# Kernel optimization log

Hardware: AMD Instinct MI355X
Metric: run time of the kernel (lower is better)

Reference implementation:

```python
import jax, jax.numpy as jnp
import numpy as np

B, L, D, H, P = 8, 1024, 128, 128, 8
W = 2 * L  # total words
FT = 0.1   # forget-gate floor


def _lin_init(k, out_d, in_d):
    k1, k2 = jax.random.split(k)
    s = 1.0 / np.sqrt(in_d)
    Wm = jax.random.uniform(k1, (out_d, in_d), minval=-s, maxval=s, dtype=jnp.float32)
    b = jax.random.uniform(k2, (out_d,), minval=-s, maxval=s, dtype=jnp.float32)
    return Wm, b


def setup_inputs() -> dict:
    key = jax.random.key(0)
    ks = jax.random.split(key, 32)
    inp = {
        "word_span0": jax.random.normal(ks[0], (B, L, D), dtype=jnp.float32),
        "word_span1": jax.random.normal(ks[1], (B, L, D), dtype=jnp.float32),
        "node_hidden": jax.random.normal(ks[2], (B, D), dtype=jnp.float32),
        "op_embedding": jax.random.normal(ks[3], (B, P, D), dtype=jnp.float32),
        "word_exist_sequence": jax.random.uniform(ks[4], (B, W), dtype=jnp.float32),
        "word_exist_matrix": jax.random.uniform(ks[5], (B, W, W), dtype=jnp.float32),
        "word_operator": jax.random.uniform(ks[6], (B, W, P), dtype=jnp.float32),
        "word_word": jax.random.uniform(ks[7], (B, W, W), dtype=jnp.float32),
        "depend0": jax.random.uniform(ks[8], (B, L, L), dtype=jnp.float32),
        "depend1": jax.random.uniform(ks[9], (B, L, L), dtype=jnp.float32),
        "goal_word": jax.random.uniform(ks[10], (B, W), dtype=jnp.float32),
    }
    dims = [("w_w_s", H, D), ("w_w_k", H, D), ("w_update", D, 3 * H),
            ("g_w", H, D), ("w_o", D, D), ("b2u_forget", D, 3 * H + D),
            ("b2u_forget2", D, 2 * D), ("linear_output", D, D),
            ("o_w", H, D), ("w_g", D, D), ("u2b_forget", D, 2 * D),
            ("w_o_forget", P, D + P * D), ("w_o_rel", P, D + P * D),
            ("w_o_update", P, 2 * P)]
    for i, (nm, o, ii) in enumerate(dims):
        Wm, b = _lin_init(ks[11 + i], o, ii)
        inp[nm + "_W"] = Wm
        inp[nm + "_b"] = b
    return inp


def _lin(x, Wm, b):
    return x @ Wm.T + b


def _nrm(m):
    # row-normalize by count of nonzero entries (torch normalize_matrix)
    return m / ((m != 0).sum(-1, keepdims=True).astype(m.dtype) + 1e-30)


def _l2(x):
    return x / (jnp.linalg.norm(x, axis=-1, keepdims=True) + 1e-30)


def _hgcn(span0, span1, node_hidden, op_emb, wes, wem, w_op, ww, dep0, dep1, gw, p):
    # ---- Bottom2Up ----
    all_word = jnp.concatenate([span0, span1], axis=1)              # [B,W,D]
    goal_trans = _lin(node_hidden, p["g_w_W"], p["g_w_b"])[:, None, :]  # [B,1,H]
    word_g = _l2(goal_trans * gw[..., None])                        # [B,W,H]
    wk_trans = _lin(all_word, p["w_w_k_W"], p["w_w_k_b"])           # [B,W,H]
    word_w_k = _l2(_nrm(ww * wem) @ wk_trans)                       # [B,W,H]
    word_w_s = _l2(jnp.concatenate(
        [_nrm(dep0) @ _lin(span0, p["w_w_s_W"], p["w_w_s_b"]),
         _nrm(dep1) @ _lin(span1, p["w_w_s_W"], p["w_w_s_b"])], axis=1))
    neighbor = jnp.concatenate([word_g, word_w_k, word_w_s], axis=-1)  # [B,W,3H]
    forget = jax.nn.sigmoid(_lin(jnp.concatenate([all_word, word_g, word_w_k, word_w_s], axis=-1),
                                 p["b2u_forget_W"], p["b2u_forget_b"]))
    word_updated = jnp.clip(forget, FT) * all_word + (1 - forget) * jax.nn.relu(
        _lin(neighbor, p["w_update_W"], p["w_update_b"]))           # [B,W,D]
    word_op = _nrm(jnp.swapaxes(wes[..., None] * w_op, 1, 2)) @ _lin(
        word_updated, p["w_o_W"], p["w_o_b"])                       # [B,P,D]
    forget2 = jax.nn.sigmoid(_lin(jnp.concatenate([op_emb, word_op], axis=-1),
                                  p["b2u_forget2_W"], p["b2u_forget2_b"]))
    op_emb = jnp.clip(forget2, FT) * op_emb + (1 - forget2) * jax.nn.relu(
        _lin(word_op, p["linear_output_W"], p["linear_output_b"]))  # [B,P,D]

    # ---- update_graph ----
    awe_n = _l2(word_updated)
    op_n = _l2(op_emb).reshape(op_emb.shape[0], -1)                 # [B,P*D]
    concate = jnp.concatenate(
        [awe_n, jnp.broadcast_to(op_n[:, None, :], (awe_n.shape[0], awe_n.shape[1], op_n.shape[-1]))],
        axis=-1)                                                    # [B,W,D+P*D]
    fg = jnp.clip(jax.nn.sigmoid(_lin(concate, p["w_o_forget_W"], p["w_o_forget_b"])), FT)
    upd = jax.nn.softmax(jax.nn.relu(_lin(
        jnp.concatenate([w_op, _lin(concate, p["w_o_rel_W"], p["w_o_rel_b"])], axis=-1),
        p["w_o_update_W"], p["w_o_update_b"])), axis=-1)
    w_op_new = fg * w_op + (1 - fg) * upd                           # [B,W,P]

    # ---- Up2Bottom ----
    span0u, span1u = word_updated[:, :L], word_updated[:, L:]
    word_o = _l2(w_op_new @ _lin(op_emb, p["o_w_W"], p["o_w_b"]))   # [B,W,H]
    word_w_k2 = _l2(_nrm(ww * wem) @ _lin(word_updated, p["w_w_k_W"], p["w_w_k_b"]))
    word_w_s2 = _l2(jnp.concatenate(
        [_nrm(dep0) @ _lin(span0u, p["w_w_s_W"], p["w_w_s_b"]),
         _nrm(dep1) @ _lin(span1u, p["w_w_s_W"], p["w_w_s_b"])], axis=1))
    neighbor2 = jnp.concatenate([word_o, word_w_k2, word_w_s2], axis=-1)
    word_updated2 = jax.nn.relu(_lin(neighbor2, p["w_update_W"], p["w_update_b"]))  # [B,W,D]
    goal_w = jnp.einsum('bw,bwd->bd', _nrm(gw * wes), word_updated2)  # [B,D]
    goal_updated = jax.nn.relu(_lin(goal_w, p["w_g_W"], p["w_g_b"]))
    fg3 = jax.nn.sigmoid(_lin(jnp.concatenate([goal_w, node_hidden], axis=-1),
                              p["u2b_forget_W"], p["u2b_forget_b"]))
    goal_next = jnp.clip(fg3, FT) * node_hidden + (1 - fg3) * goal_updated
    return (span0u, span1u, op_emb, goal_next)


def reference(word_span0, word_span1, node_hidden, op_embedding, word_exist_sequence,
              word_exist_matrix, word_operator, word_word, depend0, depend1, goal_word,
              w_w_s_W, w_w_s_b, w_w_k_W, w_w_k_b, w_update_W, w_update_b,
              g_w_W, g_w_b, w_o_W, w_o_b, b2u_forget_W, b2u_forget_b,
              b2u_forget2_W, b2u_forget2_b, linear_output_W, linear_output_b,
              o_w_W, o_w_b, w_g_W, w_g_b, u2b_forget_W, u2b_forget_b,
              w_o_forget_W, w_o_forget_b, w_o_rel_W, w_o_rel_b, w_o_update_W, w_o_update_b):
    p = dict(w_w_s_W=w_w_s_W, w_w_s_b=w_w_s_b, w_w_k_W=w_w_k_W, w_w_k_b=w_w_k_b,
             w_update_W=w_update_W, w_update_b=w_update_b, g_w_W=g_w_W, g_w_b=g_w_b,
             w_o_W=w_o_W, w_o_b=w_o_b, b2u_forget_W=b2u_forget_W, b2u_forget_b=b2u_forget_b,
             b2u_forget2_W=b2u_forget2_W, b2u_forget2_b=b2u_forget2_b,
             linear_output_W=linear_output_W, linear_output_b=linear_output_b,
             o_w_W=o_w_W, o_w_b=o_w_b, w_g_W=w_g_W, w_g_b=w_g_b,
             u2b_forget_W=u2b_forget_W, u2b_forget_b=u2b_forget_b,
             w_o_forget_W=w_o_forget_W, w_o_forget_b=w_o_forget_b,
             w_o_rel_W=w_o_rel_W, w_o_rel_b=w_o_rel_b,
             w_o_update_W=w_o_update_W, w_o_update_b=w_o_update_b)
    return _hgcn(word_span0, word_span1, node_hidden, op_embedding, word_exist_sequence,
                 word_exist_matrix, word_operator, word_word, depend0, depend1, goal_word, p)
```

## Files before the change

### kernel.cpp

```cpp
#include <hip/hip_runtime.h>

constexpr int Bn = 8, Ln = 1024, Dn = 128, Pn = 8, Wn = 2048;
constexpr float FTc = 0.1f;
constexpr int BLDc = Bn * Ln * Dn;
constexpr int BWDc = Bn * Wn * Dn;
constexpr int IDM = 1 << 28;

struct __align__(16) F4 { float v[4]; };

typedef __attribute__((ext_vector_type(8))) __bf16 bf16x8;
typedef __attribute__((ext_vector_type(8))) short short8v;
typedef __attribute__((ext_vector_type(4))) short short4v;
typedef __attribute__((ext_vector_type(4))) float f32x4;

static __device__ __forceinline__ float sigm(float x) { return 1.f / (1.f + expf(-x)); }

static __device__ __forceinline__ short f2bf(float f) {
    unsigned u = __builtin_bit_cast(unsigned, f);
    unsigned r = (u + 0x7FFFu + ((u >> 16) & 1u)) >> 16;
    return (short)r;
}

template<int NSRC, int ACT, int OUT, int BM>
__global__ __launch_bounds__(256)
void linmfma(const short* __restrict__ x0, const short* __restrict__ x1,
             const short* __restrict__ x2, const short* __restrict__ x3,
             const float* __restrict__ Wt, const float* __restrict__ bias,
             float* __restrict__ Y, short* __restrict__ Yh, short* __restrict__ Xblk,
             int in_mod, int in_stride, int in_off,
             int out_mod, int out_stride, int out_off,
             const float* __restrict__ fbuf, const float* __restrict__ bbuf)
{
    constexpr int K = NSRC * 128;
    constexpr int NKB = K / 64;
    constexpr int WRr = BM / 16;
    constexpr int WC = 4 / WRr;
    constexpr int NF = 8 / WC;
    constexpr int CPW = 128 / WC;
    __shared__ short sX[BM * 72];
    __shared__ short sW[128 * 72];

    const int tid = threadIdx.x;
    const int wave = tid >> 6, lane = tid & 63;
    const int l15 = lane & 15, l4 = lane >> 4;
    const int rg = wave % WRr, cg = wave / WRr;
    const int n0 = blockIdx.x * BM;
    const int inRow0  = (n0 / in_mod)  * in_stride  + (n0 % in_mod)  + in_off;
    const int outRow0 = (n0 / out_mod) * out_stride + (n0 % out_mod) + out_off;

    f32x4 acc[NF];
    #pragma unroll
    for (int nf = 0; nf < NF; ++nf) acc[nf] = (f32x4){0.f, 0.f, 0.f, 0.f};

    const int xrow = tid >> 3, xk8 = (tid & 7) * 8;

    for (int kb = 0; kb < NKB; ++kb) {
        const int k0 = kb * 64;
        __syncthreads();
        if (tid < BM * 8) {
            const short* __restrict__ src;
            { int s = k0 >> 7; src = (s == 0) ? x0 : (s == 1) ? x1 : (s == 2) ? x2 : x3; }
            const int koff = k0 & 127;
            *(short8v*)&sX[xrow * 72 + xk8] =
                *(const short8v*)(src + (size_t)(inRow0 + xrow) * 128 + koff + xk8);
        }
        #pragma unroll
        for (int it = 0; it < 4; ++it) {
            int idx = tid + it * 256;
            int m = idx >> 3, k8 = (idx & 7) * 8;
            const float* pw = Wt + (size_t)m * K + k0 + k8;
            F4 v0 = *(const F4*)pw, v1 = *(const F4*)(pw + 4);
            short8v sv;
            #pragma unroll
            for (int e = 0; e < 4; ++e) { sv[e] = f2bf(v0.v[e]); sv[4 + e] = f2bf(v1.v[e]); }
            *(short8v*)&sW[m * 72 + k8] = sv;
        }
        __syncthreads();
        #pragma unroll
        for (int ksub = 0; ksub < 2; ++ksub) {
            bf16x8 af = *(const bf16x8*)&sX[(rg * 16 + l15) * 72 + ksub * 32 + l4 * 8];
            #pragma unroll
            for (int nf = 0; nf < NF; ++nf) {
                bf16x8 bv = *(const bf16x8*)&sW[(cg * CPW + nf * 16 + l15) * 72 + ksub * 32 + l4 * 8];
                acc[nf] = __builtin_amdgcn_mfma_f32_16x16x32_bf16(af, bv, acc[nf], 0, 0, 0);
            }
        }
    }

    const int r0 = rg * 16 + l4 * 4;
    float vals[NF][4];
    #pragma unroll
    for (int nf = 0; nf < NF; ++nf) {
        int col = cg * CPW + nf * 16 + l15;
        float bs = bias[col];
        #pragma unroll
        for (int r = 0; r < 4; ++r) {
            int row = outRow0 + r0 + r;
            float v = acc[nf][r] + bs;
            if constexpr (ACT == 1) v = fmaxf(v, 0.f);
            if constexpr (ACT == 2) v = sigm(v);
            if constexpr (ACT == 3) {
                float f = fbuf[(size_t)row * 128 + col];
                float base = bbuf[(size_t)row * 128 + col];
                v = fmaxf(f, FTc) * base + (1.f - f) * fmaxf(v, 0.f);
            }
            vals[nf][r] = v;
            if constexpr (OUT & 1) Y[(size_t)row * 128 + col] = v;
            if constexpr (OUT & 2) Yh[(size_t)row * 128 + col] = f2bf(v);
        }
    }
    if constexpr (OUT & 4) {
        short* sS = sW;
        __syncthreads();
        #pragma unroll
        for (int nf = 0; nf < NF; ++nf) {
            int col = cg * CPW + nf * 16 + l15;
            #pragma unroll
            for (int r = 0; r < 4; ++r)
                sS[col * 40 + r0 + r] = f2bf(vals[nf][r]);
        }
        __syncthreads();
        const int bb = outRow0 >> 11, kbo = (outRow0 & 2047) >> 5;
        short* __restrict__ dst = Xblk + ((size_t)(bb * 64 + kbo)) * 4096;
        #pragma unroll
        for (int it = 0; it < 2; ++it) {
            int t2 = tid + it * 256;
            int col = t2 >> 2, k8 = (t2 & 3) * 8;
            *(short8v*)(dst + (size_t)t2 * 8) = *(const short8v*)&sS[col * 40 + k8];
        }
    }
}

template<int AMODE, int BM, bool WRA>
__global__ __launch_bounds__(512)
void mfma_gemm2(const float* __restrict__ A0, const float* __restrict__ A1,
                const short* __restrict__ Abf, short* __restrict__ Awr,
                const short* __restrict__ Xblk, short* __restrict__ Yh,
                int NI, int KJ, int xkb0, int ybs, int yoff)
{
    constexpr int WR = BM / 16;
    constexpr int WC = 4 / WR;
    constexpr int NF = 8 / WC;
    constexpr int CPW = 128 / WC;
    __shared__ short sA[2][BM * 72];
    __shared__ short sB[2][128 * 72];
    __shared__ float srow[WC][BM];

    const int tid = threadIdx.x;
    const int wave = tid >> 6, lane = tid & 63;
    const int l15 = lane & 15, l4 = lane >> 4;
    const int kg = wave >> 2;
    const int sub = wave & 3;
    const int rg = (WR == 2) ? (sub >> 1) : 0;
    const int cg = (WR == 2) ? (sub & 1) : sub;
    const int half = tid >> 8;
    const int th = tid & 255;
    const int b = blockIdx.y;
    const int i0 = blockIdx.x * BM;
    const size_t aBase = ((size_t)b * NI + i0) * KJ;
    const int KH = KJ >> 1;
    const int nkb = KH >> 6;
    const int kofs = half * KH;
    const int cbase = b * 64 + xkb0 + half * (KH >> 5);

    const int arow = th >> 3, ak16 = (th & 7) * 8, ak8 = (th & 3) * 8;

    f32x4 acc[NF];
    #pragma unroll
    for (int nf = 0; nf < NF; ++nf) acc[nf] = (f32x4){0.f, 0.f, 0.f, 0.f};

    short8v ra;
    F4 rav0, rav1, raw0, raw1;
    short8v rb0, rb1, rb2, rb3;

#define LOADA(KB)                                                              \
    if (th < BM * 8) {                                                         \
        size_t aoff = aBase + (size_t)arow * KJ + kofs + (KB)*64 + ak16;       \
        if constexpr (AMODE == 2) {                                            \
            ra = *(const short8v*)(Abf + aoff);                                \
        } else {                                                               \
            rav0 = *(const F4*)(A0 + aoff); rav1 = *(const F4*)(A0 + aoff + 4);\
            if constexpr (AMODE == 1) {                                        \
                raw0 = *(const F4*)(A1 + aoff); raw1 = *(const F4*)(A1 + aoff + 4); \
            }                                                                  \
        }                                                                      \
    }
#define STOREA(KB)                                                             \
    if (th < BM * 8) {                                                         \
        short8v sv;                                                            \
        if constexpr (AMODE == 2) { sv = ra; }                                 \
        else {                                                                 \
            _Pragma("unroll")                                                  \
            for (int e = 0; e < 4; ++e) {                                      \
                float f0 = rav0.v[e], f1 = rav1.v[e];                          \
                if constexpr (AMODE == 1) { f0 *= raw0.v[e]; f1 *= raw1.v[e]; }\
                sv[e] = f2bf(f0); sv[4 + e] = f2bf(f1);                        \
            }                                                                  \
        }                                                                      \
        *(short8v*)&sA[half][arow * 72 + ak16] = sv;                           \
        if constexpr (WRA)                                                     \
            *(short8v*)(Awr + aBase + (size_t)arow * KJ + kofs + (KB)*64 + ak16) = sv; \
    }
#define LOADB(KB)                                                              \
    {                                                                          \
        const short* s0 = Xblk + ((size_t)(cbase + (KB)*2)) * 4096;            \
        rb0 = *(const short8v*)(s0 + (size_t)th * 8);                          \
        rb1 = *(const short8v*)(s0 + (size_t)(th + 256) * 8);                  \
        rb2 = *(const short8v*)(s0 + 4096 + (size_t)th * 8);                   \
        rb3 = *(const short8v*)(s0 + 4096 + (size_t)(th + 256) * 8);           \
    }
#define STOREB()                                                               \
    {                                                                          \
        int c0 = th >> 2;             int c1 = (th + 256) >> 2;                \
        *(short8v*)&sB[half][c0 * 72 + ak8]      = rb0;                        \
        *(short8v*)&sB[half][c1 * 72 + ak8]      = rb1;                        \
        *(short8v*)&sB[half][c0 * 72 + 32 + ak8] = rb2;                        \
        *(short8v*)&sB[half][c1 * 72 + 32 + ak8] = rb3;                        \
    }

    LOADA(0); LOADB(0);
    STOREA(0); STOREB();
    __syncthreads();

    for (int kb = 0; kb < nkb; ++kb) {
        const bool more = (kb + 1 < nkb);
        if (more) { LOADA(kb + 1); LOADB(kb + 1); }
        #pragma unroll
        for (int ksub = 0; ksub < 2; ++ksub) {
            bf16x8 af = *(const bf16x8*)&sA[kg][(rg * 16 + l15) * 72 + ksub * 32 + l4 * 8];
            #pragma unroll
            for (int nf = 0; nf < NF; ++nf) {
                bf16x8 bv = *(const bf16x8*)&sB[kg][(cg * CPW + nf * 16 + l15) * 72 + ksub * 32 + l4 * 8];
                acc[nf] = __builtin_amdgcn_mfma_f32_16x16x32_bf16(af, bv, acc[nf], 0, 0, 0);
            }
        }
        if (more) {
            __syncthreads();
            STOREA(kb + 1); STOREB();
            __syncthreads();
        }
    }
#undef LOADA
#undef STOREA
#undef LOADB
#undef STOREB

    float* sC = (float*)&sB[0][0];
    __syncthreads();
    if (kg == 1) {
        #pragma unroll
        for (int nf = 0; nf < NF; ++nf)
            #pragma unroll
            for (int r = 0; r < 4; ++r)
                sC[(rg * 16 + l4 * 4 + r) * 132 + cg * CPW + nf * 16 + l15] = acc[nf][r];
    }
    __syncthreads();
    float s[4];
    if (kg == 0) {
        #pragma unroll
        for (int nf = 0; nf < NF; ++nf)
            #pragma unroll
            for (int r = 0; r < 4; ++r)
                acc[nf][r] += sC[(rg * 16 + l4 * 4 + r) * 132 + cg * CPW + nf * 16 + l15];
        #pragma unroll
        for (int r = 0; r < 4; ++r) {
            float t = 0.f;
            #pragma unroll
            for (int nf = 0; nf < NF; ++nf) t += acc[nf][r] * acc[nf][r];
            t += __shfl_xor(t, 1); t += __shfl_xor(t, 2);
            t += __shfl_xor(t, 4); t += __shfl_xor(t, 8);
            s[r] = t;
        }
        if (l15 == 0) {
            #pragma unroll
            for (int r = 0; r < 4; ++r) srow[cg][rg * 16 + l4 * 4 + r] = s[r];
        }
    }
    __syncthreads();
    if (kg == 0) {
        const int rbase = b * ybs + yoff + i0 + rg * 16 + l4 * 4;
        #pragma unroll
        for (int r = 0; r < 4; ++r) {
            float tot = 0.f;
            #pragma unroll
            for (int c = 0; c < WC; ++c) tot += srow[c][rg * 16 + l4 * 4 + r];
            float inv = 1.f / (sqrtf(tot) + 1e-30f);
            #pragma unroll
            for (int nf = 0; nf < NF; ++nf)
                Yh[(size_t)(rbase + r) * 128 + cg * CPW + nf * 16 + l15] = f2bf(acc[nf][r] * inv);
        }
    }
}

__global__ void k_allword(const float* __restrict__ s0, const float* __restrict__ s1,
                          float* __restrict__ aw, short* __restrict__ awh)
{
    int i = blockIdx.x * 256 + threadIdx.x;
    int b = i / (Ln * Dn / 4);
    F4 v0 = ((const F4*)s0)[i];
    F4 v1 = ((const F4*)s1)[i];
    int d0 = i + b * (Ln * Dn / 4);
    int d1 = i + (b + 1) * (Ln * Dn / 4);
    ((F4*)aw)[d0] = v0;
    ((F4*)aw)[d1] = v1;
    short4v h0, h1;
    #pragma unroll
    for (int e = 0; e < 4; ++e) { h0[e] = f2bf(v0.v[e]); h1[e] = f2bf(v1.v[e]); }
    ((short4v*)awh)[d0] = h0;
    ((short4v*)awh)[d1] = h1;
}

__global__ void k_goalg(const float* __restrict__ node, const float* __restrict__ Wg,
                        const float* __restrict__ bg, float* __restrict__ gvec,
                        float* __restrict__ gnorm)
{
    int b = blockIdx.x, h = threadIdx.x;
    float s = bg[h];
    for (int k = 0; k < 128; ++k) s += node[b * 128 + k] * Wg[h * 128 + k];
    gvec[b * 128 + h] = s;
    __shared__ float red[128];
    red[h] = s * s; __syncthreads();
    for (int st = 64; st > 0; st >>= 1) { if (h < st) red[h] += red[h + st]; __syncthreads(); }
    if (h == 0) gnorm[b] = sqrtf(red[0]);
}

__global__ void k_wordg(const float* __restrict__ gvec, const float* __restrict__ gnorm,
                        const float* __restrict__ gw, short* __restrict__ wgh)
{
    int row = blockIdx.x; int b = row >> 11; int h = threadIdx.x;
    float s = gw[row];
    float coef = s / (s * gnorm[b] + 1e-30f);
    wgh[(size_t)row * 128 + h] = f2bf(gvec[b * 128 + h] * coef);
}

__global__ __launch_bounds__(256)
void k_wordop_part(const float* __restrict__ wes, const float* __restrict__ wopr,
                   const float* __restrict__ Yl, float* __restrict__ part,
                   float* __restrict__ pcnt)
{
    int c = blockIdx.x, b = blockIdx.y;
    int w0 = c * 32;
    __shared__ float sc[32][8];
    int tid = threadIdx.x;
    {
        int w = tid >> 3, p = tid & 7;
        sc[w][p] = wes[b * Wn + w0 + w] * wopr[(size_t)(b * Wn + w0 + w) * Pn + p];
    }
    __syncthreads();
    if (tid < 8) {
        float n = 0.f;
        for (int w = 0; w < 32; ++w) n += (sc[w][tid] != 0.f) ? 1.f : 0.f;
        pcnt[(c * 8 + b) * 8 + tid] = n;
    }
    int d = tid & 127, g = tid >> 7;
    float acc[4] = {};
    for (int w = 0; w < 32; ++w) {
        float y = Yl[(size_t)(b * Wn + w0 + w) * 128 + d];
        #pragma unroll
        for (int q = 0; q < 4; ++q) acc[q] += sc[w][g * 4 + q] * y;
    }
    #pragma unroll
    for (int q = 0; q < 4; ++q)
        part[(((size_t)c * 8 + b) * 8 + g * 4 + q) * 128 + d] = acc[q];
}

__global__ void k_wordop_fin(const float* __restrict__ part, const float* __restrict__ pcnt,
                             float* __restrict__ outp)
{
    int bp = blockIdx.x;
    int b = bp >> 3, p = bp & 7;
    int d = threadIdx.x;
    float s = 0.f, n = 0.f;
    for (int c = 0; c < 64; ++c) s += part[(((size_t)c * 8 + b) * 8 + p) * 128 + d];
    for (int c = 0; c < 64; ++c) n += pcnt[(c * 8 + b) * 8 + p];
    outp[(size_t)bp * 128 + d] = s / (n + 1e-30f);
}

__global__ void k_opemb(const float* __restrict__ oein, const float* __restrict__ wop,
                        const float* __restrict__ W2, const float* __restrict__ b2,
                        const float* __restrict__ Wlo, const float* __restrict__ blo,
                        float* __restrict__ opembN, float* __restrict__ out2)
{
    int bp = blockIdx.x; int h = threadIdx.x;
    const float* oe = oein + (size_t)bp * 128;
    const float* wo = wop + (size_t)bp * 128;
    float s = b2[h], lo = blo[h];
    for (int k = 0; k < 128; ++k) {
        s += oe[k] * W2[h * 256 + k];
        s += wo[k] * W2[h * 256 + 128 + k];
        lo += wo[k] * Wlo[h * 128 + k];
    }
    float f = sigm(s);
    float v = fmaxf(f, FTc) * oe[h] + (1.f - f) * fmaxf(lo, 0.f);
    opembN[bp * 128 + h] = v;
    out2[bp * 128 + h] = v;
}

__global__ void k_opn(const float* __restrict__ opembN, float* __restrict__ opn)
{
    __shared__ float red[128];
    int bp = blockIdx.x, h = threadIdx.x;
    float v = opembN[bp * 128 + h];
    red[h] = v * v; __syncthreads();
    for (int s = 64; s > 0; s >>= 1) { if (h < s) red[h] += red[h + s]; __syncthreads(); }
    opn[bp * 128 + h] = v / (sqrtf(red[0]) + 1e-30f);
}

__global__ void k_cfrel(const float* __restrict__ opn, const float* __restrict__ Wf,
                        const float* __restrict__ bf, const float* __restrict__ Wr,
                        const float* __restrict__ br, float* __restrict__ cf,
                        float* __restrict__ crel)
{
    int bp = blockIdx.x; int b = bp >> 3, p = bp & 7;
    int t = threadIdx.x;
    float sf = 0.f, sr = 0.f;
    for (int k = t; k < 1024; k += 256) {
        float o = opn[b * 1024 + k];
        sf += o * Wf[p * 1152 + 128 + k];
        sr += o * Wr[p * 1152 + 128 + k];
    }
    __shared__ float rf[256], rr[256];
    rf[t] = sf; rr[t] = sr; __syncthreads();
    for (int s = 128; s > 0; s >>= 1) {
        if (t < s) { rf[t] += rf[t + s]; rr[t] += rr[t + s]; }
        __syncthreads();
    }
    if (t == 0) { cf[bp] = rf[0] + bf[p]; crel[bp] = rr[0] + br[p]; }
}

__global__ __launch_bounds__(256)
void k_fgrel(const float* __restrict__ wupd, const float* __restrict__ Wf,
             const float* __restrict__ Wr, const float* __restrict__ cf,
             const float* __restrict__ crel, float* __restrict__ fgb,
             float* __restrict__ relb)
{
    __shared__ float sXr[32 * 132];
    __shared__ float sinv[32];
    int tid = threadIdx.x;
    int n0 = blockIdx.x * 32;
    for (int l = tid; l < 4096; l += 256) {
        int r = l >> 7, h = l & 127;
        sXr[r * 132 + h] = wupd[(size_t)(n0 + r) * 128 + h];
    }
    __syncthreads();
    if (tid < 32) {
        float s = 0.f;
        for (int h = 0; h < 128; ++h) { float v = sXr[tid * 132 + h]; s += v * v; }
        sinv[tid] = 1.f / (sqrtf(s) + 1e-30f);
    }
    __syncthreads();
    int r = tid >> 3, p = tid & 7;
    int n = n0 + r; int b = n >> 11;
    float af = 0.f, ar = 0.f, inv = sinv[r];
    for (int d = 0; d < 128; ++d) {
        float x = sXr[r * 132 + d] * inv;
        af += x * Wf[p * 1152 + d];
        ar += x * Wr[p * 1152 + d];
    }
    float f = sigm(af + cf[b * 8 + p]);
    fgb[(size_t)n * 8 + p] = fmaxf(f, FTc);
    relb[(size_t)n * 8 + p] = ar + crel[b * 8 + p];
}

__global__ void k_wopnew(const float* __restrict__ wopr, const float* __restrict__ fgb,
                         const float* __restrict__ relb, const float* __restrict__ Wu,
                         const float* __restrict__ bu, float* __restrict__ wopn)
{
    int row = blockIdx.x * 256 + threadIdx.x;
    float t16[16];
    #pragma unroll
    for (int p = 0; p < 8; ++p) t16[p] = wopr[(size_t)row * 8 + p];
    #pragma unroll
    for (int p = 0; p < 8; ++p) t16[8 + p] = relb[(size_t)row * 8 + p];
    float u[8]; float m = -1e30f;
    #pragma unroll
    for (int p = 0; p < 8; ++p) {
        float s = bu[p];
        #pragma unroll
        for (int q = 0; q < 16; ++q) s += Wu[p * 16 + q] * t16[q];
        s = fmaxf(s, 0.f); u[p] = s; m = fmaxf(m, s);
    }
    float tot = 0.f;
    #pragma unroll
    for (int p = 0; p < 8; ++p) { u[p] = expf(u[p] - m); tot += u[p]; }
    float itot = 1.f / tot;
    #pragma unroll
    for (int p = 0; p < 8; ++p) {
        float f = fgb[(size_t)row * 8 + p];
        wopn[(size_t)row * 8 + p] = f * t16[p] + (1.f - f) * u[p] * itot;
    }
}

__global__ void k_opw(const float* __restrict__ opembN, const float* __restrict__ Wo,
                      const float* __restrict__ bo, float* __restrict__ opw)
{
    int bp = blockIdx.x, h = threadIdx.x;
    float s = bo[h];
    for (int d = 0; d < 128; ++d) s += opembN[bp * 128 + d] * Wo[h * 128 + d];
    opw[bp * 128 + h] = s;
}

__global__ void k_wordo(const float* __restrict__ wopn, const float* __restrict__ opw,
                        short* __restrict__ woh)
{
    int row = blockIdx.x; int b = row >> 11; int h = threadIdx.x;
    float c[8];
    #pragma unroll
    for (int p = 0; p < 8; ++p) c[p] = wopn[(size_t)row * 8 + p];
    float v = 0.f;
    #pragma unroll
    for (int p = 0; p < 8; ++p) v += c[p] * opw[(b * 8 + p) * 128 + h];
    __shared__ float red[128];
    red[h] = v * v; __syncthreads();
    for (int s = 64; s > 0; s >>= 1) { if (h < s) red[h] += red[h + s]; __syncthreads(); }
    woh[(size_t)row * 128 + h] = f2bf(v / (sqrtf(red[0]) + 1e-30f));
}

__global__ __launch_bounds__(256)
void k_goalw_part(const float* __restrict__ gw, const float* __restrict__ wes,
                  const float* __restrict__ wupd2, float* __restrict__ part,
                  float* __restrict__ pcnt)
{
    int c = blockIdx.x, b = blockIdx.y;
    int w0 = c * 32;
    __shared__ float sc[32];
    __shared__ float sa[256];
    int tid = threadIdx.x;
    if (tid < 32) sc[tid] = gw[b * Wn + w0 + tid] * wes[b * Wn + w0 + tid];
    __syncthreads();
    if (tid == 0) {
        float n = 0.f;
        for (int w = 0; w < 32; ++w) n += (sc[w] != 0.f) ? 1.f : 0.f;
        pcnt[c * 8 + b] = n;
    }
    int d = tid & 127, h = tid >> 7;
    float acc = 0.f;
    for (int w = h; w < 32; w += 2)
        acc += sc[w] * wupd2[(size_t)(b * Wn + w0 + w) * 128 + d];
    sa[tid] = acc; __syncthreads();
    if (h == 0) part[((size_t)c * 8 + b) * 128 + d] = sa[d] + sa[128 + d];
}

__global__ void k_goalw_fin(const float* __restrict__ part, const float* __restrict__ pcnt,
                            float* __restrict__ goalw)
{
    int b = blockIdx.x, d = threadIdx.x;
    float s = 0.f, n = 0.f;
    for (int c = 0; c < 64; ++c) s += part[((size_t)c * 8 + b) * 128 + d];
    for (int c = 0; c < 64; ++c) n += pcnt[c * 8 + b];
    goalw[b * 128 + d] = s / (n + 1e-30f);
}

__global__ void k_goalnext(const float* __restrict__ goalw, const float* __restrict__ node,
                           const float* __restrict__ Wg, const float* __restrict__ bg,
                           const float* __restrict__ Wu2, const float* __restrict__ bu2,
                           float* __restrict__ outg)
{
    int b = blockIdx.x, h = threadIdx.x;
    float su = bg[h], sf = bu2[h];
    for (int k = 0; k < 128; ++k) {
        float g = goalw[b * 128 + k];
        su += g * Wg[h * 128 + k];
        sf += g * Wu2[h * 256 + k] + node[b * 128 + k] * Wu2[h * 256 + 128 + k];
    }
    float gu = fmaxf(su, 0.f);
    float f = sigm(sf);
    outg[b * 128 + h] = fmaxf(f, FTc) * node[b * 128 + h] + (1.f - f) * gu;
}

__global__ void k_copyspans(const float* __restrict__ wupd, float* __restrict__ out)
{
    int i = blockIdx.x * 256 + threadIdx.x;
    F4 v = ((const F4*)wupd)[i];
    int row = i >> 5;
    int col = i & 31;
    int b = row >> 11, w = row & 2047;
    int dst;
    if (w < Ln) dst = ((b * Ln + w) << 5) + col;
    else        dst = (BLDc >> 2) + ((b * Ln + (w - Ln)) << 5) + col;
    ((F4*)out)[dst] = v;
}

extern "C" void kernel_launch(void* const* d_in, const int* in_sizes, int n_in,
                              void* d_out, int out_size, void* d_ws, size_t ws_size,
                              hipStream_t stream)
{
    const float* span0 = (const float*)d_in[0];
    const float* span1 = (const float*)d_in[1];
    const float* node  = (const float*)d_in[2];
    const float* opemb = (const float*)d_in[3];
    const float* wes   = (const float*)d_in[4];
    const float* wem   = (const float*)d_in[5];
    const float* wopr  = (const float*)d_in[6];
    const float* ww    = (const float*)d_in[7];
    const float* dep0  = (const float*)d_in[8];
    const float* dep1  = (const float*)d_in[9];
    const float* gw    = (const float*)d_in[10];
    const float* wws_W = (const float*)d_in[11]; const float* wws_b = (const float*)d_in[12];
    const float* wwk_W = (const float*)d_in[13]; const float* wwk_b = (const float*)d_in[14];
    const float* wup_W = (const float*)d_in[15]; const float* wup_b = (const float*)d_in[16];
    const float* gw_W  = (const float*)d_in[17]; const float* gw_b  = (const float*)d_in[18];
    const float* wo_W  = (const float*)d_in[19]; const float* wo_b  = (const float*)d_in[20];
    const float* bf_W  = (const float*)d_in[21]; const float* bf_b  = (const float*)d_in[22];
    const float* bf2_W = (const float*)d_in[23]; const float* bf2_b = (const float*)d_in[24];
    const float* lo_W  = (const float*)d_in[25]; const float* lo_b  = (const float*)d_in[26];
    const float* ow_W  = (const float*)d_in[27]; const float* ow_b  = (const float*)d_in[28];
    const float* wg_W  = (const float*)d_in[29]; const float* wg_b  = (const float*)d_in[30];
    const float* u2b_W = (const float*)d_in[31]; const float* u2b_b = (const float*)d_in[32];
    const float* wof_W = (const float*)d_in[33]; const float* wof_b = (const float*)d_in[34];
    const float* wor_W = (const float*)d_in[35]; const float* wor_b = (const float*)d_in[36];
    const float* wou_W = (const float*)d_in[37]; const float* wou_b = (const float*)d_in[38];

    float* out = (float*)d_out;
    float* out_op   = out + 2 * BLDc;
    float* out_goal = out + 2 * BLDc + Bn * Pn * Dn;

    float* ws = (float*)d_ws;
    float* allword = ws;
    float* wupd    = ws + 1 * BWDc;
    float* tmpA    = ws + 2 * BWDc;
    float* tmpB    = ws + 3 * BWDc;
    float* sm      = ws + 4 * BWDc;
    float* gvec   = sm;
    float* gnorm  = sm + 1024;
    float* wordop = sm + 1056;
    float* opembN = sm + 9248;
    float* opn    = sm + 17440;
    float* cf     = sm + 25632;
    float* crel   = sm + 25696;
    float* opw    = sm + 25760;
    float* goalw  = sm + 33952;
    float* fgb    = sm + 34976;
    float* relb   = sm + 166048;
    float* wopn   = sm + 297120;

    short* allwordh = (short*)(ws + 4 * (size_t)BWDc + 458752);
    short* wupdh  = allwordh + BWDc;
    short* wordgh = wupdh + BWDc;
    short* wwkh   = wordgh + BWDc;
    short* wwsh   = wwkh + BWDc;
    short* Xblk   = wwsh + BWDc;
    short* Awwem  = Xblk + BWDc;
    short* dep0b  = Awwem + (size_t)Bn * Wn * Wn;
    short* dep1b  = dep0b + (size_t)Bn * Ln * Ln;

    const dim3 blk(256);
    const dim3 blk512(512);

    k_allword<<<1024, blk, 0, stream>>>(span0, span1, allword, allwordh);
    linmfma<1,0,4,32><<<512, blk, 0, stream>>>(allwordh, nullptr, nullptr, nullptr,
        wwk_W, wwk_b, nullptr, nullptr, Xblk, IDM, 0, 0, IDM, 0, 0, nullptr, nullptr);
    mfma_gemm2<1,32,true><<<dim3(64, 8), blk512, 0, stream>>>(ww, wem, nullptr, Awwem,
        Xblk, wwkh, Wn, Wn, 0, Wn, 0);
    linmfma<1,0,4,32><<<256, blk, 0, stream>>>(allwordh, nullptr, nullptr, nullptr,
        wws_W, wws_b, nullptr, nullptr, Xblk, Ln, Wn, 0, Ln, Wn, 0, nullptr, nullptr);
    linmfma<1,0,4,32><<<256, blk, 0, stream>>>(allwordh, nullptr, nullptr, nullptr,
        wws_W, wws_b, nullptr, nullptr, Xblk, Ln, Wn, Ln, Ln, Wn, Ln, nullptr, nullptr);
    mfma_gemm2<0,16,true><<<dim3(64, 8), blk512, 0, stream>>>(dep0, nullptr, nullptr, dep0b,
        Xblk, wwsh, Ln, Ln, 0, Wn, 0);
    mfma_gemm2<0,16,true><<<dim3(64, 8), blk512, 0, stream>>>(dep1, nullptr, nullptr, dep1b,
        Xblk, wwsh, Ln, Ln, 32, Wn, Ln);
    k_goalg<<<8, 128, 0, stream>>>(node, gw_W, gw_b, gvec, gnorm);
    k_wordg<<<16384, 128, 0, stream>>>(gvec, gnorm, gw, wordgh);
    linmfma<4,2,1,16><<<1024, blk, 0, stream>>>(allwordh, wordgh, wwkh, wwsh,
        bf_W, bf_b, tmpB, nullptr, nullptr, IDM, 0, 0, IDM, 0, 0, nullptr, nullptr);
    linmfma<3,3,3,16><<<1024, blk, 0, stream>>>(wordgh, wwkh, wwsh, nullptr,
        wup_W, wup_b, wupd, wupdh, nullptr, IDM, 0, 0, IDM, 0, 0, tmpB, allword);
    linmfma<1,0,1,16><<<1024, blk, 0, stream>>>(wupdh, nullptr, nullptr, nullptr,
        wo_W, wo_b, tmpA, nullptr, nullptr, IDM, 0, 0, IDM, 0, 0, nullptr, nullptr);
    k_wordop_part<<<dim3(64, 8), blk, 0, stream>>>(wes, wopr, tmpA, tmpB, tmpB + 524288);
    k_wordop_fin<<<64, 128, 0, stream>>>(tmpB, tmpB + 524288, wordop);
    k_opemb<<<64, 128, 0, stream>>>(opemb, wordop, bf2_W, bf2_b, lo_W, lo_b, opembN, out_op);
    k_opn<<<64, 128, 0, stream>>>(opembN, opn);
    k_cfrel<<<64, blk, 0, stream>>>(opn, wof_W, wof_b, wor_W, wor_b, cf, crel);
    k_fgrel<<<512, blk, 0, stream>>>(wupd, wof_W, wor_W, cf, crel, fgb, relb);
    k_wopnew<<<64, blk, 0, stream>>>(wopr, fgb, relb, wou_W, wou_b, wopn);
    k_opw<<<64, 128, 0, stream>>>(opembN, ow_W, ow_b, opw);
    k_wordo<<<16384, 128, 0, stream>>>(wopn, opw, wordgh);

    linmfma<1,0,4,32><<<512, blk, 0, stream>>>(wupdh, nullptr, nullptr, nullptr,
        wwk_W, wwk_b, nullptr, nullptr, Xblk, IDM, 0, 0, IDM, 0, 0, nullptr, nullptr);
    mfma_gemm2<2,32,false><<<dim3(64, 8), blk512, 0, stream>>>(nullptr, nullptr, Awwem, nullptr,
        Xblk, wwkh, Wn, Wn, 0, Wn, 0);
    linmfma<1,0,4,32><<<256, blk, 0, stream>>>(wupdh, nullptr, nullptr, nullptr,
        wws_W, wws_b, nullptr, nullptr, Xblk, Ln, Wn, 0, Ln, Wn, 0, nullptr, nullptr);
    linmfma<1,0,4,32><<<256, blk, 0, stream>>>(wupdh, nullptr, nullptr, nullptr,
        wws_W, wws_b, nullptr, nullptr, Xblk, Ln, Wn, Ln, Ln, Wn, Ln, nullptr, nullptr);
    mfma_gemm2<2,16,false><<<dim3(64, 8), blk512, 0, stream>>>(nullptr, nullptr, dep0b, nullptr,
        Xblk, wwsh, Ln, Ln, 0, Wn, 0);
    mfma_gemm2<2,16,false><<<dim3(64, 8), blk512, 0, stream>>>(nullptr, nullptr, dep1b, nullptr,
        Xblk, wwsh, Ln, Ln, 32, Wn, Ln);
    linmfma<3,1,1,16><<<1024, blk, 0, stream>>>(wordgh, wwkh, wwsh, nullptr,
        wup_W, wup_b, tmpA, nullptr, nullptr, IDM, 0, 0, IDM, 0, 0, nullptr, nullptr);
    k_goalw_part<<<dim3(64, 8), blk, 0, stream>>>(gw, wes, tmpA, tmpB, tmpB + 65536);
    k_goalw_fin<<<8, 128, 0, stream>>>(tmpB, tmpB + 65536, goalw);
    k_goalnext<<<8, 128, 0, stream>>>(goalw, node, wg_W, wg_b, u2b_W, u2b_b, out_goal);
    k_copyspans<<<2048, blk, 0, stream>>>(wupd, out);
}
```

Baseline: 356.8 us.

## Fuse wwk/wws projections, drop fp32 allword copy and span copy kernel

Adds a lin2x kernel that computes the wwk and wws projections from the same bf16 input tile in one pass, writing both blocked outputs into separate buffers (reusing tmpA/tmpB as scratch). This replaces three linmfma launches per stage. The fp32 allword buffer is removed: the update epilogue now reads span0/span1 directly and also writes the final output spans, which removes the k_copyspans kernel. In exchange there is an extra scattered store in the update epilogue, and tmpA/tmpB are now aliased as Xblk scratch, so their lifetimes must not overlap.

```diff
diff --git a/kernel.cpp b/kernel.cpp
--- a/kernel.cpp
+++ b/kernel.cpp
@@ -26,10 +26,11 @@
 void linmfma(const short* __restrict__ x0, const short* __restrict__ x1,
              const short* __restrict__ x2, const short* __restrict__ x3,
              const float* __restrict__ Wt, const float* __restrict__ bias,
-             float* __restrict__ Y, short* __restrict__ Yh, short* __restrict__ Xblk,
+             float* __restrict__ Y, short* __restrict__ Yh,
              int in_mod, int in_stride, int in_off,
              int out_mod, int out_stride, int out_off,
-             const float* __restrict__ fbuf, const float* __restrict__ bbuf)
+             const float* __restrict__ fbuf, const float* __restrict__ bbuf0,
+             const float* __restrict__ bbuf1, float* __restrict__ outs)
 {
     constexpr int K = NSRC * 128;
     constexpr int NKB = K / 64;
@@ -88,7 +89,6 @@
     }
 
     const int r0 = rg * 16 + l4 * 4;
-    float vals[NF][4];
     #pragma unroll
     for (int nf = 0; nf < NF; ++nf) {
         int col = cg * CPW + nf * 16 + l15;
@@ -100,33 +100,108 @@
             if constexpr (ACT == 1) v = fmaxf(v, 0.f);
             if constexpr (ACT == 2) v = sigm(v);
             if constexpr (ACT == 3) {
+                int bw = row & 2047, bb = row >> 11;
+                const float* bp = (bw < Ln) ? bbuf0 : bbuf1;
+                float base = bp[(size_t)((bb << 10) + (bw & 1023)) * 128 + col];
                 float f = fbuf[(size_t)row * 128 + col];
-                float base = bbuf[(size_t)row * 128 + col];
                 v = fmaxf(f, FTc) * base + (1.f - f) * fmaxf(v, 0.f);
-            }
-            vals[nf][r] = v;
+                if constexpr (OUT & 8) {
+                    int drow = (bw < Ln) ? (bb * Ln + bw) : (8192 + bb * Ln + (bw - Ln));
+                    outs[(size_t)drow * 128 + col] = v;
+                }
+            }
             if constexpr (OUT & 1) Y[(size_t)row * 128 + col] = v;
             if constexpr (OUT & 2) Yh[(size_t)row * 128 + col] = f2bf(v);
         }
     }
-    if constexpr (OUT & 4) {
-        short* sS = sW;
+}
+
+__global__ __launch_bounds__(256)
+void lin2x(const short* __restrict__ x0,
+           const float* __restrict__ W0, const float* __restrict__ b0v,
+           const float* __restrict__ W1, const float* __restrict__ b1v,
+           short* __restrict__ Xout0, short* __restrict__ Xout1)
+{
+    __shared__ short sX[32 * 72];
+    __shared__ short sW[2][128 * 72];
+    const int tid = threadIdx.x;
+    const int wave = tid >> 6, lane = tid & 63;
+    const int l15 = lane & 15, l4 = lane >> 4;
+    const int rg = wave & 1, cg = wave >> 1;
+    const int n0 = blockIdx.x * 32;
+
+    f32x4 acc[2][4];
+    #pragma unroll
+    for (int o = 0; o < 2; ++o) {
+        #pragma unroll
+        for (int nf = 0; nf < 4; ++nf) {
+            acc[o][nf] = (f32x4){0.f, 0.f, 0.f, 0.f};
+        }
+    }
+
+    const int xrow = tid >> 3, xk8 = (tid & 7) * 8;
+
+    #pragma unroll
+    for (int kb = 0; kb < 2; ++kb) {
+        const int k0 = kb * 64;
         __syncthreads();
-        #pragma unroll
-        for (int nf = 0; nf < NF; ++nf) {
-            int col = cg * CPW + nf * 16 + l15;
-            #pragma unroll
-            for (int r = 0; r < 4; ++r)
-                sS[col * 40 + r0 + r] = f2bf(vals[nf][r]);
+        *(short8v*)&sX[xrow * 72 + xk8] =
+            *(const short8v*)(x0 + (size_t)(n0 + xrow) * 128 + k0 + xk8);
+        #pragma unroll
+        for (int o = 0; o < 2; ++o) {
+            const float* __restrict__ Wt = o ? W1 : W0;
+            #pragma unroll
+            for (int it = 0; it < 4; ++it) {
+                int idx = tid + it * 256;
+                int m = idx >> 3, k8 = (idx & 7) * 8;
+                const float* pw = Wt + (size_t)m * 128 + k0 + k8;
+                F4 v0 = *(const F4*)pw, v1 = *(const F4*)(pw + 4);
+                short8v sv;
+                #pragma unroll
+                for (int e = 0; e < 4; ++e) { sv[e] = f2bf(v0.v[e]); sv[4 + e] = f2bf(v1.v[e]); }
+                *(short8v*)&sW[o][m * 72 + k8] = sv;
+            }
         }
         __syncthreads();
-        const int bb = outRow0 >> 11, kbo = (outRow0 & 2047) >> 5;
-        short* __restrict__ dst = Xblk + ((size_t)(bb * 64 + kbo)) * 4096;
+        #pragma unroll
+        for (int ksub = 0; ksub < 2; ++ksub) {
+            bf16x8 af = *(const bf16x8*)&sX[(rg * 16 + l15) * 72 + ksub * 32 + l4 * 8];
+            #pragma unroll
+            for (int o = 0; o < 2; ++o) {
+                #pragma unroll
+                for (int nf = 0; nf < 4; ++nf) {
+                    bf16x8 bv = *(const bf16x8*)&sW[o][(cg * 64 + nf * 16 + l15) * 72 + ksub * 32 + l4 * 8];
+                    acc[o][nf] = __builtin_amdgcn_mfma_f32_16x16x32_bf16(af, bv, acc[o][nf], 0, 0, 0);
+                }
+            }
+        }
+    }
+
+    const int r0 = rg * 16 + l4 * 4;
+    __syncthreads();
+    #pragma unroll
+    for (int o = 0; o < 2; ++o) {
+        const float* bv = o ? b1v : b0v;
+        #pragma unroll
+        for (int nf = 0; nf < 4; ++nf) {
+            int col = cg * 64 + nf * 16 + l15;
+            float bs = bv[col];
+            #pragma unroll
+            for (int r = 0; r < 4; ++r) {
+                sW[o][col * 40 + r0 + r] = f2bf(acc[o][nf][r] + bs);
+            }
+        }
+    }
+    __syncthreads();
+    const int bb = n0 >> 11, kbo = (n0 & 2047) >> 5;
+    #pragma unroll
+    for (int o = 0; o < 2; ++o) {
+        short* __restrict__ dst = (o ? Xout1 : Xout0) + ((size_t)(bb * 64 + kbo)) * 4096;
         #pragma unroll
         for (int it = 0; it < 2; ++it) {
             int t2 = tid + it * 256;
             int col = t2 >> 2, k8 = (t2 & 3) * 8;
-            *(short8v*)(dst + (size_t)t2 * 8) = *(const short8v*)&sS[col * 40 + k8];
+            *(short8v*)(dst + (size_t)t2 * 8) = *(const short8v*)&sW[o][col * 40 + k8];
         }
     }
 }
@@ -249,19 +324,23 @@
     __syncthreads();
     if (kg == 1) {
         #pragma unroll
-        for (int nf = 0; nf < NF; ++nf)
-            #pragma unroll
-            for (int r = 0; r < 4; ++r)
+        for (int nf = 0; nf < NF; ++nf) {
+            #pragma unroll
+            for (int r = 0; r < 4; ++r) {
                 sC[(rg * 16 + l4 * 4 + r) * 132 + cg * CPW + nf * 16 + l15] = acc[nf][r];
+            }
+        }
     }
     __syncthreads();
     float s[4];
     if (kg == 0) {
         #pragma unroll
-        for (int nf = 0; nf < NF; ++nf)
-            #pragma unroll
-            for (int r = 0; r < 4; ++r)
+        for (int nf = 0; nf < NF; ++nf) {
+            #pragma unroll
+            for (int r = 0; r < 4; ++r) {
                 acc[nf][r] += sC[(rg * 16 + l4 * 4 + r) * 132 + cg * CPW + nf * 16 + l15];
+            }
+        }
         #pragma unroll
         for (int r = 0; r < 4; ++r) {
             float t = 0.f;
@@ -286,14 +365,15 @@
             for (int c = 0; c < WC; ++c) tot += srow[c][rg * 16 + l4 * 4 + r];
             float inv = 1.f / (sqrtf(tot) + 1e-30f);
             #pragma unroll
-            for (int nf = 0; nf < NF; ++nf)
+            for (int nf = 0; nf < NF; ++nf) {
                 Yh[(size_t)(rbase + r) * 128 + cg * CPW + nf * 16 + l15] = f2bf(acc[nf][r] * inv);
-        }
-    }
-}
-
-__global__ void k_allword(const float* __restrict__ s0, const float* __restrict__ s1,
-                          float* __restrict__ aw, short* __restrict__ awh)
+            }
+        }
+    }
+}
+
+__global__ void k_allwordh(const float* __restrict__ s0, const float* __restrict__ s1,
+                           short* __restrict__ awh)
 {
     int i = blockIdx.x * 256 + threadIdx.x;
     int b = i / (Ln * Dn / 4);
@@ -301,8 +381,6 @@
     F4 v1 = ((const F4*)s1)[i];
     int d0 = i + b * (Ln * Dn / 4);
     int d1 = i + (b + 1) * (Ln * Dn / 4);
-    ((F4*)aw)[d0] = v0;
-    ((F4*)aw)[d1] = v1;
     short4v h0, h1;
     #pragma unroll
     for (int e = 0; e < 4; ++e) { h0[e] = f2bf(v0.v[e]); h1[e] = f2bf(v1.v[e]); }
@@ -566,19 +644,6 @@
     float gu = fmaxf(su, 0.f);
     float f = sigm(sf);
     outg[b * 128 + h] = fmaxf(f, FTc) * node[b * 128 + h] + (1.f - f) * gu;
-}
-
-__global__ void k_copyspans(const float* __restrict__ wupd, float* __restrict__ out)
-{
-    int i = blockIdx.x * 256 + threadIdx.x;
-    F4 v = ((const F4*)wupd)[i];
-    int row = i >> 5;
-    int col = i & 31;
-    int b = row >> 11, w = row & 2047;
-    int dst;
-    if (w < Ln) dst = ((b * Ln + w) << 5) + col;
-    else        dst = (BLDc >> 2) + ((b * Ln + (w - Ln)) << 5) + col;
-    ((F4*)out)[dst] = v;
 }
 
 extern "C" void kernel_launch(void* const* d_in, const int* in_sizes, int n_in,
@@ -616,11 +681,10 @@
     float* out_goal = out + 2 * BLDc + Bn * Pn * Dn;
 
     float* ws = (float*)d_ws;
-    float* allword = ws;
-    float* wupd    = ws + 1 * BWDc;
-    float* tmpA    = ws + 2 * BWDc;
-    float* tmpB    = ws + 3 * BWDc;
-    float* sm      = ws + 4 * BWDc;
+    float* wupd    = ws;
+    float* tmpA    = ws + 1 * BWDc;
+    float* tmpB    = ws + 2 * BWDc;
+    float* sm      = ws + 3 * BWDc;
     float* gvec   = sm;
     float* gnorm  = sm + 1024;
     float* wordop = sm + 1056;
@@ -634,7 +698,7 @@
     float* relb   = sm + 166048;
     float* wopn   = sm + 297120;
 
-    short* allwordh = (short*)(ws + 4 * (size_t)BWDc + 458752);
+    short* allwordh = (short*)(ws + 3 * (size_t)BWDc + 458752);
     short* wupdh  = allwordh + BWDc;
     short* wordgh = wupdh + BWDc;
     short* wwkh   = wordgh + BWDc;
@@ -644,30 +708,28 @@
     short* dep0b  = Awwem + (size_t)Bn * Wn * Wn;
     short* dep1b  = dep0b + (size_t)Bn * Ln * Ln;
 
+    short* XblkS1 = (short*)tmpA;
+    short* XblkS2 = (short*)tmpB;
+
     const dim3 blk(256);
     const dim3 blk512(512);
 
-    k_allword<<<1024, blk, 0, stream>>>(span0, span1, allword, allwordh);
-    linmfma<1,0,4,32><<<512, blk, 0, stream>>>(allwordh, nullptr, nullptr, nullptr,
-        wwk_W, wwk_b, nullptr, nullptr, Xblk, IDM, 0, 0, IDM, 0, 0, nullptr, nullptr);
+    k_allwordh<<<1024, blk, 0, stream>>>(span0, span1, allwordh);
+    lin2x<<<512, blk, 0, stream>>>(allwordh, wwk_W, wwk_b, wws_W, wws_b, Xblk, XblkS1);
     mfma_gemm2<1,32,true><<<dim3(64, 8), blk512, 0, stream>>>(ww, wem, nullptr, Awwem,
         Xblk, wwkh, Wn, Wn, 0, Wn, 0);
-    linmfma<1,0,4,32><<<256, blk, 0, stream>>>(allwordh, nullptr, nullptr, nullptr,
-        wws_W, wws_b, nullptr, nullptr, Xblk, Ln, Wn, 0, Ln, Wn, 0, nullptr, nullptr);
-    linmfma<1,0,4,32><<<256, blk, 0, stream>>>(allwordh, nullptr, nullptr, nullptr,
-        wws_W, wws_b, nullptr, nullptr, Xblk, Ln, Wn, Ln, Ln, Wn, Ln, nullptr, nullptr);
     mfma_gemm2<0,16,true><<<dim3(64, 8), blk512, 0, stream>>>(dep0, nullptr, nullptr, dep0b,
-        Xblk, wwsh, Ln, Ln, 0, Wn, 0);
+        XblkS1, wwsh, Ln, Ln, 0, Wn, 0);
     mfma_gemm2<0,16,true><<<dim3(64, 8), blk512, 0, stream>>>(dep1, nullptr, nullptr, dep1b,
-        Xblk, wwsh, Ln, Ln, 32, Wn, Ln);
+        XblkS1, wwsh, Ln, Ln, 32, Wn, Ln);
     k_goalg<<<8, 128, 0, stream>>>(node, gw_W, gw_b, gvec, gnorm);
     k_wordg<<<16384, 128, 0, stream>>>(gvec, gnorm, gw, wordgh);
     linmfma<4,2,1,16><<<1024, blk, 0, stream>>>(allwordh, wordgh, wwkh, wwsh,
-        bf_W, bf_b, tmpB, nullptr, nullptr, IDM, 0, 0, IDM, 0, 0, nullptr, nullptr);
-    linmfma<3,3,3,16><<<1024, blk, 0, stream>>>(wordgh, wwkh, wwsh, nullptr,
-        wup_W, wup_b, wupd, wupdh, nullptr, IDM, 0, 0, IDM, 0, 0, tmpB, allword);
+        bf_W, bf_b, tmpB, nullptr, IDM, 0, 0, IDM, 0, 0, nullptr, nullptr, nullptr, nullptr);
+    linmfma<3,3,11,16><<<1024, blk, 0, stream>>>(wordgh, wwkh, wwsh, nullptr,
+        wup_W, wup_b, wupd, wupdh, IDM, 0, 0, IDM, 0, 0, tmpB, span0, span1, out);
     linmfma<1,0,1,16><<<1024, blk, 0, stream>>>(wupdh, nullptr, nullptr, nullptr,
-        wo_W, wo_b, tmpA, nullptr, nullptr, IDM, 0, 0, IDM, 0, 0, nullptr, nullptr);
+        wo_W, wo_b, tmpA, nullptr, IDM, 0, 0, IDM, 0, 0, nullptr, nullptr, nullptr, nullptr);
     k_wordop_part<<<dim3(64, 8), blk, 0, stream>>>(wes, wopr, tmpA, tmpB, tmpB + 524288);
     k_wordop_fin<<<64, 128, 0, stream>>>(tmpB, tmpB + 524288, wordop);
     k_opemb<<<64, 128, 0, stream>>>(opemb, wordop, bf2_W, bf2_b, lo_W, lo_b, opembN, out_op);
@@ -678,22 +740,16 @@
     k_opw<<<64, 128, 0, stream>>>(opembN, ow_W, ow_b, opw);
     k_wordo<<<16384, 128, 0, stream>>>(wopn, opw, wordgh);
 
-    linmfma<1,0,4,32><<<512, blk, 0, stream>>>(wupdh, nullptr, nullptr, nullptr,
-        wwk_W, wwk_b, nullptr, nullptr, Xblk, IDM, 0, 0, IDM, 0, 0, nullptr, nullptr);
+    lin2x<<<512, blk, 0, stream>>>(wupdh, wwk_W, wwk_b, wws_W, wws_b, Xblk, XblkS2);
     mfma_gemm2<2,32,false><<<dim3(64, 8), blk512, 0, stream>>>(nullptr, nullptr, Awwem, nullptr,
         Xblk, wwkh, Wn, Wn, 0, Wn, 0);
-    linmfma<1,0,4,32><<<256, blk, 0, stream>>>(wupdh, nullptr, nullptr, nullptr,
-        wws_W, wws_b, nullptr, nullptr, Xblk, Ln, Wn, 0, Ln, Wn, 0, nullptr, nullptr);
-    linmfma<1,0,4,32><<<256, blk, 0, stream>>>(wupdh, nullptr, nullptr, nullptr,
-        wws_W, wws_b, nullptr, nullptr, Xblk, Ln, Wn, Ln, Ln, Wn, Ln, nullptr, nullptr);
     mfma_gemm2<2,16,false><<<dim3(64, 8), blk512, 0, stream>>>(nullptr, nullptr, dep0b, nullptr,
-        Xblk, wwsh, Ln, Ln, 0, Wn, 0);
+        XblkS2, wwsh, Ln, Ln, 0, Wn, 0);
     mfma_gemm2<2,16,false><<<dim3(64, 8), blk512, 0, stream>>>(nullptr, nullptr, dep1b, nullptr,
-        Xblk, wwsh, Ln, Ln, 32, Wn, Ln);
+        XblkS2, wwsh, Ln, Ln, 32, Wn, Ln);
     linmfma<3,1,1,16><<<1024, blk, 0, stream>>>(wordgh, wwkh, wwsh, nullptr,
-        wup_W, wup_b, tmpA, nullptr, nullptr, IDM, 0, 0, IDM, 0, 0, nullptr, nullptr);
+        wup_W, wup_b, tmpA, nullptr, IDM, 0, 0, IDM, 0, 0, nullptr, nullptr, nullptr, nullptr);
     k_goalw_part<<<dim3(64, 8), blk, 0, stream>>>(gw, wes, tmpA, tmpB, tmpB + 65536);
     k_goalw_fin<<<8, 128, 0, stream>>>(tmpB, tmpB + 65536, goalw);
     k_goalnext<<<8, 128, 0, stream>>>(goalw, node, wg_W, wg_b, u2b_W, u2b_b, out_goal);
-    k_copyspans<<<2048, blk, 0, stream>>>(wupd, out);
-}
+}
```

New measurement: 339.1 us. 5.0% less time.
